# Performance work log

Measured on AMD Instinct MI355X. Metric: run time of the kernel, lower is better.

The kernel has to match this reference:

```python
import jax, jax.numpy as jnp
import numpy as np

WEIGHT_SP = 0.1
BANDWIDTH = 0.5
EPS = 1e-5


def _l2_normalize(v, axis, eps=1e-12):
    # matches torch F.normalize(p=2): x / max(||x||, eps)
    n = jnp.sqrt(jnp.sum(v * v, axis=axis, keepdims=True))
    return v / jnp.maximum(n, eps)


def _compute_meshgrid(N, H, W):
    rows = jnp.arange(H, dtype=jnp.float32) / (H + 1)
    cols = jnp.arange(W, dtype=jnp.float32) / (W + 1)
    gr, gc = jnp.meshgrid(rows, cols, indexing="ij")
    grid = jnp.stack([gr, gc])[None]  # (1, 2, H, W)
    return jnp.broadcast_to(grid, (N, 2, H, W))


def _l2_distance(x, y):
    # Faithful to the torch code; its broadcasting is only valid for N == 1.
    N, C, H, W = x.shape
    xv = x.reshape(N, C, -1)
    yv = y.reshape(N, C, -1)
    x_s = jnp.sum(xv ** 2, axis=1)          # (N, HW)
    y_s = jnp.sum(yv ** 2, axis=1)          # (N, HW)
    A = jnp.einsum("nci,ncj->nij", yv, xv)  # (N, HW, HW)
    dist = y_s - 2.0 * A + x_s.T            # same broadcast as torch (N==1)
    dist = jnp.swapaxes(dist, 1, 2)         # transpose(1,2); reshape is no-op
    return jnp.maximum(dist, 0.0)


def _cosine_distance(x, y):
    y_mu = jnp.mean(y, axis=(0, 2, 3), keepdims=True)   # (1, C, 1, 1)
    xn = _l2_normalize(x - y_mu, axis=1)
    yn = _l2_normalize(y - y_mu, axis=1)
    N, C = x.shape[:2]
    xn = xn.reshape(N, C, -1)
    yn = yn.reshape(N, C, -1)
    cos = jnp.einsum("nci,ncj->nij", xn, yn)            # (N, HW, HW)
    return 1.0 - cos


def _relative_distance(dist, eps=1e-5):
    dmin = jnp.min(dist, axis=2, keepdims=True)
    return dist / (dmin + eps)


def _compute_cx(dist_tilde, bandwidth):
    w = jnp.exp((1.0 - dist_tilde) / bandwidth)
    return w / jnp.sum(w, axis=2, keepdims=True)


def setup_inputs() -> dict:
    key = jax.random.key(0)
    k1, k2 = jax.random.split(key)
    x = jax.random.normal(k1, (1, 512, 80, 80), dtype=jnp.float32)
    y = jax.random.normal(k2, (1, 512, 80, 80), dtype=jnp.float32)
    return {"x": x, "y": y}


def reference(x, y):
    N, C, H, W = x.shape
    # spatial branch
    grid = _compute_meshgrid(N, H, W)
    cx_sp = _compute_cx(_relative_distance(_l2_distance(grid, grid), 1e-5), BANDWIDTH)
    # feature branch (loss_type == 'cosine')
    cx_feat = _compute_cx(_relative_distance(_cosine_distance(x, y), EPS), BANDWIDTH)
    cx_combine = (1.0 - WEIGHT_SP) * cx_feat + WEIGHT_SP * cx_sp
    k_max = jnp.max(cx_combine, axis=2, keepdims=True)  # (N, HW, 1)
    cx = jnp.mean(k_max, axis=1)                        # (N, 1)
    return jnp.mean(-jnp.log(cx + EPS))
```

## Files before the change

kernel.cpp:

```cpp
#include <hip/hip_runtime.h>
#include <hip/hip_bf16.h>
#include <math.h>

#define HW 6400
#define NC 512
#define NH 80
#define NW 80
#define NCH 25
#define NSLOT 50
#define NCYS 8
#define JCH 256
#define TI 128
#define BK 64
#define NT16 400

typedef __attribute__((ext_vector_type(8))) short short8;
typedef __attribute__((ext_vector_type(4))) float v4f;

#define MU_OFF    0
#define SQX_OFF   512
#define SQY_OFF   (512 + HW)
#define ACC_OFF   (512 + 2*HW)
#define GMAXP_OFF (ACC_OFF + 64)
#define INVD_OFF  (GMAXP_OFF + HW*NSLOT)
#define ZP_OFF    (INVD_OFF + HW)
#define WDP_OFF   (ZP_OFF + HW*NSLOT)
#define F32_FLOATS (WDP_OFF + HW*NCYS)
#define XB_BYTE   ((size_t)(((F32_FLOATS*4) + 255) & ~255))
#define YB_BYTE   (XB_BYTE + (size_t)HW*NC*2)
#define G_BYTE    (YB_BYTE + (size_t)HW*NC*2)
#define G_BYTES   ((size_t)NT16 * NT16 * 256 * 2)

typedef __attribute__((address_space(1))) unsigned int uint_g;
typedef __attribute__((address_space(3))) unsigned int uint_l;
__device__ __forceinline__ void gload16(const void* g, void* l) {
    __builtin_amdgcn_global_load_lds((const uint_g*)g, (uint_l*)l, 16, 0, 0);
}

__global__ void k_mu(const float* __restrict__ y, float* __restrict__ mu) {
    int c = blockIdx.x;
    const float* yc = y + (size_t)c * HW;
    float s = 0.f;
    for (int i = threadIdx.x; i < HW; i += 256) s += yc[i];
    __shared__ float red[256];
    red[threadIdx.x] = s;
    __syncthreads();
    for (int off = 128; off > 0; off >>= 1) {
        if (threadIdx.x < off) red[threadIdx.x] += red[threadIdx.x + off];
        __syncthreads();
    }
    if (threadIdx.x == 0) mu[c] = red[0] * (1.0f / HW);
}

__global__ void k_transpose(const float* __restrict__ x, const float* __restrict__ y,
                            const float* __restrict__ mu,
                            float* __restrict__ sqx, float* __restrict__ sqy,
                            unsigned short* __restrict__ xb, unsigned short* __restrict__ yb) {
    __shared__ float tile[64 * 68];
    const int t = threadIdx.x;
    const int i0 = blockIdx.x * 64;
    const int c0 = blockIdx.y * 64;
    const int z = blockIdx.z;
    const float* src = z ? y : x;
    float* sq = z ? sqy : sqx;
    unsigned short* dst = z ? yb : xb;

    #pragma unroll 4
    for (int it = 0; it < 16; ++it) {
        int cl = it * 4 + (t >> 6);
        int il = t & 63;
        float v = src[(size_t)(c0 + cl) * HW + i0 + il] - mu[c0 + cl];
        tile[il * 68 + cl] = v;
    }
    __syncthreads();
    {
        int il = t & 63, q = t >> 6;
        float s = 0.f;
        #pragma unroll
        for (int cl = q * 16; cl < q * 16 + 16; ++cl) {
            float v = tile[il * 68 + cl];
            s = fmaf(v, v, s);
        }
        atomicAdd(&sq[i0 + il], s);
    }
    #pragma unroll
    for (int it = 0; it < 2; ++it) {
        int il = t >> 2;
        int seg = (t & 3) + it * 4;
        unsigned int pk[4];
        #pragma unroll
        for (int p = 0; p < 4; ++p) {
            float v0 = tile[il * 68 + seg * 8 + p * 2];
            float v1 = tile[il * 68 + seg * 8 + p * 2 + 1];
            __hip_bfloat16 h0 = __float2bfloat16(v0);
            __hip_bfloat16 h1 = __float2bfloat16(v1);
            unsigned short u0 = *reinterpret_cast<unsigned short*>(&h0);
            unsigned short u1 = *reinterpret_cast<unsigned short*>(&h1);
            pk[p] = (unsigned int)u0 | ((unsigned int)u1 << 16);
        }
        uint4 val = make_uint4(pk[0], pk[1], pk[2], pk[3]);
        *(uint4*)&dst[(size_t)(i0 + il) * NC + c0 + seg * 8] = val;
    }
}

__global__ void k_normfin(float* __restrict__ sqx, float* __restrict__ sqy) {
    int i = blockIdx.x * 256 + threadIdx.x;
    sqx[i] = 1.0f / fmaxf(sqrtf(sqx[i]), 1e-12f);
    sqy[i] = 1.0f / fmaxf(sqrtf(sqy[i]), 1e-12f);
}

__device__ __forceinline__ void rmax_epilogue(float (&rmax)[16], float* gmaxp,
                                              int i0, int wr, int wc, int lr, int lg) {
    #pragma unroll
    for (int u = 0; u < 16; ++u) {
        float v = rmax[u];
        v = fmaxf(v, __shfl_xor(v, 1));
        v = fmaxf(v, __shfl_xor(v, 2));
        v = fmaxf(v, __shfl_xor(v, 4));
        v = fmaxf(v, __shfl_xor(v, 8));
        if (lr == 0) {
            int row = i0 + wr * 64 + (u >> 2) * 16 + lg * 4 + (u & 3);
            gmaxp[(size_t)row * NSLOT + blockIdx.y * 2 + wc] = v;
        }
    }
}

__global__ __launch_bounds__(256, 2) void k_pass1s(const unsigned short* __restrict__ Xb,
                                                   const unsigned short* __restrict__ Yb,
                                                   const float* __restrict__ sxi,
                                                   const float* __restrict__ syi,
                                                   float* __restrict__ gmaxp,
                                                   unsigned int* __restrict__ G2) {
    __shared__ char sA[128 * 128];
    __shared__ char sB[256 * 128];
    const int t = threadIdx.x;
    const int w = t >> 6, l = t & 63;
    const int wr = w >> 1, wc = w & 1;
    const int lr = l & 15, lg = l >> 4;
    const int i0 = blockIdx.x * TI;
    const int jbase = blockIdx.y * JCH;

    int aoff[4][2], boff[8][2];
    #pragma unroll
    for (int mt = 0; mt < 4; ++mt) {
        int row = wr * 64 + mt * 16 + lr;
        #pragma unroll
        for (int ks = 0; ks < 2; ++ks) {
            int seg = ks * 4 + lg;
            aoff[mt][ks] = row * 128 + ((seg ^ (row & 7)) * 16);
        }
    }
    #pragma unroll
    for (int nt = 0; nt < 8; ++nt) {
        int row = wc * 128 + nt * 16 + lr;
        #pragma unroll
        for (int ks = 0; ks < 2; ++ks) {
            int seg = ks * 4 + lg;
            boff[nt][ks] = row * 128 + ((seg ^ (row & 7)) * 16);
        }
    }

    const int strow = l >> 3;
    const int stcol = ((l & 7) ^ strow) * 8;
    const unsigned short* ga = Xb + (size_t)(i0 + w * 32 + strow) * NC + stcol;
    const unsigned short* gb = Yb + (size_t)(jbase + w * 64 + strow) * NC + stcol;
    char* dA = sA + w * 4096;
    char* dB = sB + w * 8192;

    v4f acc[4][8];
    #pragma unroll
    for (int mt = 0; mt < 4; ++mt)
        #pragma unroll
        for (int nt = 0; nt < 8; ++nt)
            acc[mt][nt] = (v4f){0.f, 0.f, 0.f, 0.f};

    #pragma unroll 1
    for (int kt = 0; kt < NC; kt += BK) {
        __syncthreads();
        gload16(ga + kt,           dA);
        gload16(ga + 8  * NC + kt, dA + 1024);
        gload16(ga + 16 * NC + kt, dA + 2048);
        gload16(ga + 24 * NC + kt, dA + 3072);
        #pragma unroll
        for (int it = 0; it < 8; ++it)
            gload16(gb + it * 8 * NC + kt, dB + it * 1024);
        __syncthreads();
        #pragma unroll
        for (int ks = 0; ks < 2; ++ks) {
            short8 af[4], bf[8];
            #pragma unroll
            for (int mt = 0; mt < 4; ++mt) af[mt] = *(const short8*)&sA[aoff[mt][ks]];
            #pragma unroll
            for (int nt = 0; nt < 8; ++nt) bf[nt] = *(const short8*)&sB[boff[nt][ks]];
            #pragma unroll
            for (int mt = 0; mt < 4; ++mt)
                #pragma unroll
                for (int nt = 0; nt < 8; ++nt)
                    acc[mt][nt] = __builtin_amdgcn_mfma_f32_16x16x32_bf16(
                        af[mt], bf[nt], acc[mt][nt], 0, 0, 0);
        }
    }

    float rsx[16];
    #pragma unroll
    for (int u = 0; u < 16; ++u) {
        int row = i0 + wr * 64 + (u >> 2) * 16 + lg * 4 + (u & 3);
        rsx[u] = sxi[row];
    }
    float rsy[8];
    #pragma unroll
    for (int nt = 0; nt < 8; ++nt)
        rsy[nt] = syi[jbase + wc * 128 + nt * 16 + lr];

    float rmax[16];
    #pragma unroll
    for (int u = 0; u < 16; ++u) rmax[u] = -3.0e38f;

    #pragma unroll
    for (int mt = 0; mt < 4; ++mt) {
        size_t rbase = (size_t)(i0 / 16 + wr * 4 + mt) * (NT16 * 128);
        #pragma unroll
        for (int nt = 0; nt < 8; ++nt) {
            int ct = jbase / 16 + wc * 8 + nt;
            float g0 = acc[mt][nt][0] * rsx[mt * 4 + 0] * rsy[nt];
            float g1 = acc[mt][nt][1] * rsx[mt * 4 + 1] * rsy[nt];
            float g2 = acc[mt][nt][2] * rsx[mt * 4 + 2] * rsy[nt];
            float g3 = acc[mt][nt][3] * rsx[mt * 4 + 3] * rsy[nt];
            rmax[mt * 4 + 0] = fmaxf(rmax[mt * 4 + 0], g0);
            rmax[mt * 4 + 1] = fmaxf(rmax[mt * 4 + 1], g1);
            rmax[mt * 4 + 2] = fmaxf(rmax[mt * 4 + 2], g2);
            rmax[mt * 4 + 3] = fmaxf(rmax[mt * 4 + 3], g3);
            __hip_bfloat16 h0 = __float2bfloat16(g0);
            __hip_bfloat16 h1 = __float2bfloat16(g1);
            __hip_bfloat16 h2 = __float2bfloat16(g2);
            __hip_bfloat16 h3 = __float2bfloat16(g3);
            unsigned int pk0 = (unsigned int)*(unsigned short*)&h0 | ((unsigned int)*(unsigned short*)&h1 << 16);
            unsigned int pk1 = (unsigned int)*(unsigned short*)&h2 | ((unsigned int)*(unsigned short*)&h3 << 16);
            *(uint2*)&G2[rbase + (size_t)ct * 128 + l * 2] = make_uint2(pk0, pk1);
        }
    }
    rmax_epilogue(rmax, gmaxp, i0, wr, wc, lr, lg);
}

__global__ __launch_bounds__(256) void k_pass2s(const unsigned int* __restrict__ G2,
                                                const float* __restrict__ gmaxp,
                                                float* __restrict__ zp,
                                                float* __restrict__ wdp) {
    const int t = threadIdx.x;
    const int w = t >> 6, l = t & 63;
    const int lr = l & 15, lg = l >> 4;
    const int rt = blockIdx.x * 4 + w;
    const int cy = blockIdx.y;

    float m = -3.0e38f;
    {
        int row = rt * 16 + lr;
        #pragma unroll
        for (int k = 0; k < 13; ++k) {
            int s = lg + 4 * k;
            if (s < NSLOT) m = fmaxf(m, gmaxp[(size_t)row * NSLOT + s]);
        }
        m = fmaxf(m, __shfl_xor(m, 16));
        m = fmaxf(m, __shfl_xor(m, 32));
    }
    float inv_lr = 1.0f / ((1.0f - m) + 1e-5f);
    float c1[4], c2[4];
    #pragma unroll
    for (int r = 0; r < 4; ++r) {
        float iv = __shfl(inv_lr, lg * 4 + r);
        c2[r] = 2.0f * iv;
        c1[r] = 2.0f - 2.0f * iv;
    }

    const uint2* base = (const uint2*)G2 + (size_t)rt * (NT16 * 64) + l;
    float zs[4] = {0.f, 0.f, 0.f, 0.f};
    #pragma unroll 4
    for (int ct = cy * 50; ct < cy * 50 + 50; ++ct) {
        uint2 v = base[(size_t)ct * 64];
        float g0 = __uint_as_float((v.x & 0xFFFFu) << 16);
        float g1 = __uint_as_float(v.x & 0xFFFF0000u);
        float g2 = __uint_as_float((v.y & 0xFFFFu) << 16);
        float g3 = __uint_as_float(v.y & 0xFFFF0000u);
        zs[0] += __expf(fmaf(c2[0], g0, c1[0]));
        zs[1] += __expf(fmaf(c2[1], g1, c1[1]));
        zs[2] += __expf(fmaf(c2[2], g2, c1[2]));
        zs[3] += __expf(fmaf(c2[3], g3, c1[3]));
    }
    float wd[4] = {0.f, 0.f, 0.f, 0.f};
    if (rt / 50 == cy) {
        uint2 v = base[(size_t)rt * 64];
        float g[4];
        g[0] = __uint_as_float((v.x & 0xFFFFu) << 16);
        g[1] = __uint_as_float(v.x & 0xFFFF0000u);
        g[2] = __uint_as_float((v.y & 0xFFFFu) << 16);
        g[3] = __uint_as_float(v.y & 0xFFFF0000u);
        #pragma unroll
        for (int r = 0; r < 4; ++r)
            if (lr == lg * 4 + r) wd[r] = __expf(fmaf(c2[r], g[r], c1[r]));
    }
    #pragma unroll
    for (int r = 0; r < 4; ++r) {
        float z = zs[r], d = wd[r];
        z += __shfl_xor(z, 1);  d += __shfl_xor(d, 1);
        z += __shfl_xor(z, 2);  d += __shfl_xor(d, 2);
        z += __shfl_xor(z, 4);  d += __shfl_xor(d, 4);
        z += __shfl_xor(z, 8);  d += __shfl_xor(d, 8);
        if (lr == 0) {
            int row = rt * 16 + lg * 4 + r;
            zp[(size_t)row * NCYS + cy] = z;
            wdp[(size_t)row * NCYS + cy] = d;
        }
    }
}

__global__ void k_kmax_s(const float* __restrict__ zp, const float* __restrict__ wdp,
                         const float* __restrict__ gmaxp, float* __restrict__ accum,
                         int* __restrict__ counter, float* __restrict__ out) {
    int i = blockIdx.x * 256 + threadIdx.x;
    float Z = 0.f, wd = 0.f, gmax = -3.0e38f;
    #pragma unroll
    for (int s = 0; s < NCYS; ++s) {
        Z += zp[(size_t)i * NCYS + s];
        wd += wdp[(size_t)i * NCYS + s];
    }
    #pragma unroll
    for (int s = 0; s < NSLOT; ++s) gmax = fmaxf(gmax, gmaxp[(size_t)i * NSLOT + s]);
    float dmin = 1.0f - gmax;
    float inv = 1.0f / (dmin + 1e-5f);
    float wmx = __expf(2.0f - 2.0f * dmin * inv);
    float invZ = 1.0f / Z;
    float kmax = fmaxf(0.9f * wmx * invZ, 0.9f * wd * invZ + 0.1f);

    __shared__ float red[256];
    red[threadIdx.x] = kmax;
    __syncthreads();
    for (int off = 128; off > 0; off >>= 1) {
        if (threadIdx.x < off) red[threadIdx.x] += red[threadIdx.x + off];
        __syncthreads();
    }
    if (threadIdx.x == 0) {
        atomicAdd(accum, red[0]);
        __threadfence();
        int n = atomicAdd(counter, 1);
        if (n == (int)gridDim.x - 1) {
            float total = atomicAdd(accum, 0.0f);
            out[0] = -logf(total * (1.0f / HW) + 1e-5f);
        }
    }
}

template <typename F>
__device__ __forceinline__ void gemm_driver(const unsigned short* __restrict__ Xb,
                                            const unsigned short* __restrict__ Yb,
                                            F&& consume) {
    __shared__ char sA[TI * BK * 2];
    __shared__ char sB[TI * BK * 2];
    const int t = threadIdx.x;
    const int w = t >> 6, l = t & 63;
    const int wr = w >> 1, wc = w & 1;
    const int lr = l & 15, lg = l >> 4;
    const int i0 = blockIdx.x * TI;
    const int jbase = blockIdx.y * JCH;

    int aoff[4][2], boff[4][2];
    #pragma unroll
    for (int mt = 0; mt < 4; ++mt) {
        int row = wr * 64 + mt * 16 + lr;
        #pragma unroll
        for (int ks = 0; ks < 2; ++ks) {
            int seg = ks * 4 + lg;
            aoff[mt][ks] = row * 128 + ((seg ^ (row & 7)) * 16);
        }
    }
    #pragma unroll
    for (int nt = 0; nt < 4; ++nt) {
        int row = wc * 64 + nt * 16 + lr;
        #pragma unroll
        for (int ks = 0; ks < 2; ++ks) {
            int seg = ks * 4 + lg;
            boff[nt][ks] = row * 128 + ((seg ^ (row & 7)) * 16);
        }
    }
    const int strow = l >> 3;
    const int stcol = ((l & 7) ^ strow) * 8;
    char* dA0 = sA + (w * 4 + 0) * 1024;
    char* dA1 = sA + (w * 4 + 1) * 1024;
    char* dA2 = sA + (w * 4 + 2) * 1024;
    char* dA3 = sA + (w * 4 + 3) * 1024;
    char* dB0 = sB + (w * 4 + 0) * 1024;
    char* dB1 = sB + (w * 4 + 1) * 1024;
    char* dB2 = sB + (w * 4 + 2) * 1024;
    char* dB3 = sB + (w * 4 + 3) * 1024;
    const unsigned short* ga = Xb + (size_t)(i0 + w * 32 + strow) * NC + stcol;
    const unsigned short* gb0 = Yb + (size_t)(jbase + w * 32 + strow) * NC + stcol;

    #pragma unroll 1
    for (int jt = 0; jt < JCH; jt += TI) {
        const unsigned short* gb = gb0 + (size_t)jt * NC;
        v4f acc[4][4];
        #pragma unroll
        for (int mt = 0; mt < 4; ++mt)
            #pragma unroll
            for (int nt = 0; nt < 4; ++nt)
                acc[mt][nt] = (v4f){0.f, 0.f, 0.f, 0.f};

        #pragma unroll 1
        for (int kt = 0; kt < NC; kt += BK) {
            __syncthreads();
            gload16(ga + kt,           dA0);
            gload16(ga + 8  * NC + kt, dA1);
            gload16(ga + 16 * NC + kt, dA2);
            gload16(ga + 24 * NC + kt, dA3);
            gload16(gb + kt,           dB0);
            gload16(gb + 8  * NC + kt, dB1);
            gload16(gb + 16 * NC + kt, dB2);
            gload16(gb + 24 * NC + kt, dB3);
            __syncthreads();
            #pragma unroll
            for (int ks = 0; ks < 2; ++ks) {
                short8 af[4], bf[4];
                #pragma unroll
                for (int mt = 0; mt < 4; ++mt) af[mt] = *(const short8*)&sA[aoff[mt][ks]];
                #pragma unroll
                for (int nt = 0; nt < 4; ++nt) bf[nt] = *(const short8*)&sB[boff[nt][ks]];
                #pragma unroll
                for (int mt = 0; mt < 4; ++mt)
                    #pragma unroll
                    for (int nt = 0; nt < 4; ++nt)
                        acc[mt][nt] = __builtin_amdgcn_mfma_f32_16x16x32_bf16(
                            af[mt], bf[nt], acc[mt][nt], 0, 0, 0);
            }
        }
        consume(acc, jt);
    }
}

__global__ __launch_bounds__(256, 2) void k_pass1(const unsigned short* __restrict__ Xb,
                                                  const unsigned short* __restrict__ Yb,
                                                  const float* __restrict__ sxi,
                                                  const float* __restrict__ syi,
                                                  float* __restrict__ gmaxp) {
    const int t = threadIdx.x;
    const int w = t >> 6, l = t & 63;
    const int wr = w >> 1, wc = w & 1;
    const int lr = l & 15, lg = l >> 4;
    const int i0 = blockIdx.x * TI;
    const int jbase = blockIdx.y * JCH;
    float rsx[16], rmax[16];
    #pragma unroll
    for (int u = 0; u < 16; ++u) {
        int row = i0 + wr * 64 + (u >> 2) * 16 + lg * 4 + (u & 3);
        rsx[u] = sxi[row];
        rmax[u] = -3.0e38f;
    }
    gemm_driver(Xb, Yb, [&](v4f (&acc)[4][4], int jt) {
        #pragma unroll
        for (int nt = 0; nt < 4; ++nt) {
            float sy = syi[jbase + jt + (wc * 4 + nt) * 16 + lr];
            #pragma unroll
            for (int mt = 0; mt < 4; ++mt)
                #pragma unroll
                for (int r = 0; r < 4; ++r)
                    rmax[mt * 4 + r] = fmaxf(rmax[mt * 4 + r],
                                             acc[mt][nt][r] * rsx[mt * 4 + r] * sy);
        }
    });
    rmax_epilogue(rmax, gmaxp, i0, wr, wc, lr, lg);
}

__global__ void k_invd(const float* __restrict__ gmaxp, float* __restrict__ invd) {
    int i = blockIdx.x * 256 + threadIdx.x;
    float m = -3.0e38f;
    #pragma unroll
    for (int s = 0; s < NSLOT; ++s) m = fmaxf(m, gmaxp[(size_t)i * NSLOT + s]);
    invd[i] = 1.0f / ((1.0f - m) + 1e-5f);
}

__global__ __launch_bounds__(256, 2) void k_pass2(const unsigned short* __restrict__ Xb,
                                                  const unsigned short* __restrict__ Yb,
                                                  const float* __restrict__ sxi,
                                                  const float* __restrict__ syi,
                                                  const float* __restrict__ invd,
                                                  float* __restrict__ zp) {
    const int t = threadIdx.x;
    const int w = t >> 6, l = t & 63;
    const int wr = w >> 1, wc = w & 1;
    const int lr = l & 15, lg = l >> 4;
    const int i0 = blockIdx.x * TI;
    const int jbase = blockIdx.y * JCH;
    float zs[16], c1[16], c2[16], rsx[16];
    #pragma unroll
    for (int u = 0; u < 16; ++u) {
        int row = i0 + wr * 64 + (u >> 2) * 16 + lg * 4 + (u & 3);
        float inv = invd[row];
        c2[u] = 2.0f * inv;
        c1[u] = 2.0f - 2.0f * inv;
        rsx[u] = sxi[row];
        zs[u] = 0.f;
    }
    gemm_driver(Xb, Yb, [&](v4f (&acc)[4][4], int jt) {
        #pragma unroll
        for (int nt = 0; nt < 4; ++nt) {
            float sy = syi[jbase + jt + (wc * 4 + nt) * 16 + lr];
            #pragma unroll
            for (int mt = 0; mt < 4; ++mt)
                #pragma unroll
                for (int r = 0; r < 4; ++r) {
                    int u = mt * 4 + r;
                    float g = acc[mt][nt][r] * rsx[u] * sy;
                    zs[u] += __expf(fmaf(c2[u], g, c1[u]));
                }
        }
    });
    #pragma unroll
    for (int u = 0; u < 16; ++u) {
        float z = zs[u];
        z += __shfl_xor(z, 1);
        z += __shfl_xor(z, 2);
        z += __shfl_xor(z, 4);
        z += __shfl_xor(z, 8);
        if (lr == 0) {
            int row = i0 + wr * 64 + (u >> 2) * 16 + lg * 4 + (u & 3);
            zp[(size_t)row * NSLOT + blockIdx.y * 2 + wc] = z;
        }
    }
}

__global__ void k_kmax(const float* __restrict__ zp, const float* __restrict__ gmaxp,
                       const unsigned short* __restrict__ Xb, const unsigned short* __restrict__ Yb,
                       const float* __restrict__ sxi, const float* __restrict__ syi,
                       float* __restrict__ accum, int* __restrict__ counter,
                       float* __restrict__ out) {
    int i = blockIdx.x * 256 + threadIdx.x;
    float Z = 0.f, gmax = -3.0e38f;
    #pragma unroll
    for (int s = 0; s < NSLOT; ++s) {
        Z += zp[(size_t)i * NSLOT + s];
        gmax = fmaxf(gmax, gmaxp[(size_t)i * NSLOT + s]);
    }
    float gii = 0.f;
    const uint2* xr = (const uint2*)(Xb + (size_t)i * NC);
    const uint2* yr = (const uint2*)(Yb + (size_t)i * NC);
    for (int c4 = 0; c4 < NC / 4; ++c4) {
        uint2 xa = xr[c4], ya = yr[c4];
        float x0 = __uint_as_float((xa.x & 0xFFFFu) << 16), y0 = __uint_as_float((ya.x & 0xFFFFu) << 16);
        float x1 = __uint_as_float(xa.x & 0xFFFF0000u),     y1 = __uint_as_float(ya.x & 0xFFFF0000u);
        float x2 = __uint_as_float((xa.y & 0xFFFFu) << 16), y2 = __uint_as_float((ya.y & 0xFFFFu) << 16);
        float x3 = __uint_as_float(xa.y & 0xFFFF0000u),     y3 = __uint_as_float(ya.y & 0xFFFF0000u);
        gii = fmaf(x0, y0, gii); gii = fmaf(x1, y1, gii);
        gii = fmaf(x2, y2, gii); gii = fmaf(x3, y3, gii);
    }
    gii *= sxi[i] * syi[i];
    float dmin = 1.0f - gmax;
    float inv = 1.0f / (dmin + 1e-5f);
    float wmx = __expf(2.0f - 2.0f * dmin * inv);
    float wii = __expf(2.0f - 2.0f * (1.0f - gii) * inv);
    float invZ = 1.0f / Z;
    float kmax = fmaxf(0.9f * wmx * invZ, 0.9f * wii * invZ + 0.1f);

    __shared__ float red[256];
    red[threadIdx.x] = kmax;
    __syncthreads();
    for (int off = 128; off > 0; off >>= 1) {
        if (threadIdx.x < off) red[threadIdx.x] += red[threadIdx.x + off];
        __syncthreads();
    }
    if (threadIdx.x == 0) {
        atomicAdd(accum, red[0]);
        __threadfence();
        int n = atomicAdd(counter, 1);
        if (n == (int)gridDim.x - 1) {
            float total = atomicAdd(accum, 0.0f);
            out[0] = -logf(total * (1.0f / HW) + 1e-5f);
        }
    }
}

extern "C" void kernel_launch(void* const* d_in, const int* in_sizes, int n_in,
                              void* d_out, int out_size, void* d_ws, size_t ws_size,
                              hipStream_t stream) {
    const float* x = (const float*)d_in[0];
    const float* y = (const float*)d_in[1];
    float* out = (float*)d_out;
    float* ws = (float*)d_ws;

    float* mu    = ws + MU_OFF;
    float* sqx   = ws + SQX_OFF;
    float* sqy   = ws + SQY_OFF;
    float* accum = ws + ACC_OFF;
    int*   counter = (int*)(accum + 1);
    float* gmaxp = ws + GMAXP_OFF;
    float* invd  = ws + INVD_OFF;
    float* zp    = ws + ZP_OFF;
    float* wdp   = ws + WDP_OFF;
    unsigned short* Xb = (unsigned short*)((char*)d_ws + XB_BYTE);
    unsigned short* Yb = (unsigned short*)((char*)d_ws + YB_BYTE);
    unsigned int*   G2 = (unsigned int*)((char*)d_ws + G_BYTE);

    const bool bigws = ws_size >= (G_BYTE + G_BYTES);

    hipMemsetAsync(sqx, 0, (2 * HW + 64) * sizeof(float), stream);

    hipLaunchKernelGGL(k_mu, dim3(NC), dim3(256), 0, stream, y, mu);
    hipLaunchKernelGGL(k_transpose, dim3(HW / 64, NC / 64, 2), dim3(256), 0, stream,
                       x, y, mu, sqx, sqy, Xb, Yb);
    hipLaunchKernelGGL(k_normfin, dim3(HW / 256), dim3(256), 0, stream, sqx, sqy);

    dim3 grid(HW / TI, NCH);
    if (bigws) {
        hipLaunchKernelGGL(k_pass1s, grid, dim3(256), 0, stream, Xb, Yb, sqx, sqy, gmaxp, G2);
        hipLaunchKernelGGL(k_pass2s, dim3(NT16 / 4, NCYS), dim3(256), 0, stream, G2, gmaxp, zp, wdp);
        hipLaunchKernelGGL(k_kmax_s, dim3(HW / 256), dim3(256), 0, stream, zp, wdp, gmaxp,
                           accum, counter, out);
    } else {
        hipLaunchKernelGGL(k_pass1, grid, dim3(256), 0, stream, Xb, Yb, sqx, sqy, gmaxp);
        hipLaunchKernelGGL(k_invd, dim3(HW / 256), dim3(256), 0, stream, gmaxp, invd);
        hipLaunchKernelGGL(k_pass2, grid, dim3(256), 0, stream, Xb, Yb, sqx, sqy, invd, zp);
        hipLaunchKernelGGL(k_kmax, dim3(HW / 256), dim3(256), 0, stream, zp, gmaxp, Xb, Yb,
                           sqx, sqy, accum, counter, out);
    }
}
```

Baseline: 164.1 us.

## Store normalized Gram matrix in FP8 and fold norm finalization into GEMM

The stored similarity matrix drops from packed bf16 to packed fp8 (e4m3), halving the bytes pass1s writes and pass2s reads. The diagonal is written separately at fp32 so pass2s no longer has to compute a diagonal term. The norm-finalization kernel is removed and reciprocal norms are computed inline from the squared sums. pass1s is reworked to a 128x128 tile looped over the 256-column chunk, with launch bounds raised to 3 blocks per CU. The cost is fp8 rounding error inside the exponentials of the softmax denominator, which may hurt accuracy.

Measured after the change: 168.0 us. 2.3% more time.

```diff
diff --git a/kernel.cpp b/kernel.cpp
--- a/kernel.cpp
+++ b/kernel.cpp
@@ -22,19 +22,22 @@
 #define SQY_OFF   (512 + HW)
 #define ACC_OFF   (512 + 2*HW)
 #define GMAXP_OFF (ACC_OFF + 64)
-#define INVD_OFF  (GMAXP_OFF + HW*NSLOT)
-#define ZP_OFF    (INVD_OFF + HW)
-#define WDP_OFF   (ZP_OFF + HW*NSLOT)
-#define F32_FLOATS (WDP_OFF + HW*NCYS)
+#define GDIAG_OFF (GMAXP_OFF + HW*NSLOT)
+#define ZP_OFF    (GDIAG_OFF + HW)
+#define F32_FLOATS (ZP_OFF + HW*NSLOT)
 #define XB_BYTE   ((size_t)(((F32_FLOATS*4) + 255) & ~255))
 #define YB_BYTE   (XB_BYTE + (size_t)HW*NC*2)
 #define G_BYTE    (YB_BYTE + (size_t)HW*NC*2)
-#define G_BYTES   ((size_t)NT16 * NT16 * 256 * 2)
+#define G_BYTES   ((size_t)NT16 * NT16 * 256)
 
 typedef __attribute__((address_space(1))) unsigned int uint_g;
 typedef __attribute__((address_space(3))) unsigned int uint_l;
 __device__ __forceinline__ void gload16(const void* g, void* l) {
     __builtin_amdgcn_global_load_lds((const uint_g*)g, (uint_l*)l, 16, 0, 0);
+}
+
+__device__ __forceinline__ float rnorm_of(float sq) {
+    return 1.0f / fmaxf(sqrtf(sq), 1e-12f);
 }
 
 __global__ void k_mu(const float* __restrict__ y, float* __restrict__ mu) {
@@ -103,12 +106,6 @@
     }
 }
 
-__global__ void k_normfin(float* __restrict__ sqx, float* __restrict__ sqy) {
-    int i = blockIdx.x * 256 + threadIdx.x;
-    sqx[i] = 1.0f / fmaxf(sqrtf(sqx[i]), 1e-12f);
-    sqy[i] = 1.0f / fmaxf(sqrtf(sqy[i]), 1e-12f);
-}
-
 __device__ __forceinline__ void rmax_epilogue(float (&rmax)[16], float* gmaxp,
                                               int i0, int wr, int wc, int lr, int lg) {
     #pragma unroll
@@ -125,234 +122,13 @@
     }
 }
 
-__global__ __launch_bounds__(256, 2) void k_pass1s(const unsigned short* __restrict__ Xb,
+__global__ __launch_bounds__(256, 3) void k_pass1s(const unsigned short* __restrict__ Xb,
                                                    const unsigned short* __restrict__ Yb,
-                                                   const float* __restrict__ sxi,
-                                                   const float* __restrict__ syi,
+                                                   const float* __restrict__ sqx,
+                                                   const float* __restrict__ sqy,
                                                    float* __restrict__ gmaxp,
-                                                   unsigned int* __restrict__ G2) {
-    __shared__ char sA[128 * 128];
-    __shared__ char sB[256 * 128];
-    const int t = threadIdx.x;
-    const int w = t >> 6, l = t & 63;
-    const int wr = w >> 1, wc = w & 1;
-    const int lr = l & 15, lg = l >> 4;
-    const int i0 = blockIdx.x * TI;
-    const int jbase = blockIdx.y * JCH;
-
-    int aoff[4][2], boff[8][2];
-    #pragma unroll
-    for (int mt = 0; mt < 4; ++mt) {
-        int row = wr * 64 + mt * 16 + lr;
-        #pragma unroll
-        for (int ks = 0; ks < 2; ++ks) {
-            int seg = ks * 4 + lg;
-            aoff[mt][ks] = row * 128 + ((seg ^ (row & 7)) * 16);
-        }
-    }
-    #pragma unroll
-    for (int nt = 0; nt < 8; ++nt) {
-        int row = wc * 128 + nt * 16 + lr;
-        #pragma unroll
-        for (int ks = 0; ks < 2; ++ks) {
-            int seg = ks * 4 + lg;
-            boff[nt][ks] = row * 128 + ((seg ^ (row & 7)) * 16);
-        }
-    }
-
-    const int strow = l >> 3;
-    const int stcol = ((l & 7) ^ strow) * 8;
-    const unsigned short* ga = Xb + (size_t)(i0 + w * 32 + strow) * NC + stcol;
-    const unsigned short* gb = Yb + (size_t)(jbase + w * 64 + strow) * NC + stcol;
-    char* dA = sA + w * 4096;
-    char* dB = sB + w * 8192;
-
-    v4f acc[4][8];
-    #pragma unroll
-    for (int mt = 0; mt < 4; ++mt)
-        #pragma unroll
-        for (int nt = 0; nt < 8; ++nt)
-            acc[mt][nt] = (v4f){0.f, 0.f, 0.f, 0.f};
-
-    #pragma unroll 1
-    for (int kt = 0; kt < NC; kt += BK) {
-        __syncthreads();
-        gload16(ga + kt,           dA);
-        gload16(ga + 8  * NC + kt, dA + 1024);
-        gload16(ga + 16 * NC + kt, dA + 2048);
-        gload16(ga + 24 * NC + kt, dA + 3072);
-        #pragma unroll
-        for (int it = 0; it < 8; ++it)
-            gload16(gb + it * 8 * NC + kt, dB + it * 1024);
-        __syncthreads();
-        #pragma unroll
-        for (int ks = 0; ks < 2; ++ks) {
-            short8 af[4], bf[8];
-            #pragma unroll
-            for (int mt = 0; mt < 4; ++mt) af[mt] = *(const short8*)&sA[aoff[mt][ks]];
-            #pragma unroll
-            for (int nt = 0; nt < 8; ++nt) bf[nt] = *(const short8*)&sB[boff[nt][ks]];
-            #pragma unroll
-            for (int mt = 0; mt < 4; ++mt)
-                #pragma unroll
-                for (int nt = 0; nt < 8; ++nt)
-                    acc[mt][nt] = __builtin_amdgcn_mfma_f32_16x16x32_bf16(
-                        af[mt], bf[nt], acc[mt][nt], 0, 0, 0);
-        }
-    }
-
-    float rsx[16];
-    #pragma unroll
-    for (int u = 0; u < 16; ++u) {
-        int row = i0 + wr * 64 + (u >> 2) * 16 + lg * 4 + (u & 3);
-        rsx[u] = sxi[row];
-    }
-    float rsy[8];
-    #pragma unroll
-    for (int nt = 0; nt < 8; ++nt)
-        rsy[nt] = syi[jbase + wc * 128 + nt * 16 + lr];
-
-    float rmax[16];
-    #pragma unroll
-    for (int u = 0; u < 16; ++u) rmax[u] = -3.0e38f;
-
-    #pragma unroll
-    for (int mt = 0; mt < 4; ++mt) {
-        size_t rbase = (size_t)(i0 / 16 + wr * 4 + mt) * (NT16 * 128);
-        #pragma unroll
-        for (int nt = 0; nt < 8; ++nt) {
-            int ct = jbase / 16 + wc * 8 + nt;
-            float g0 = acc[mt][nt][0] * rsx[mt * 4 + 0] * rsy[nt];
-            float g1 = acc[mt][nt][1] * rsx[mt * 4 + 1] * rsy[nt];
-            float g2 = acc[mt][nt][2] * rsx[mt * 4 + 2] * rsy[nt];
-            float g3 = acc[mt][nt][3] * rsx[mt * 4 + 3] * rsy[nt];
-            rmax[mt * 4 + 0] = fmaxf(rmax[mt * 4 + 0], g0);
-            rmax[mt * 4 + 1] = fmaxf(rmax[mt * 4 + 1], g1);
-            rmax[mt * 4 + 2] = fmaxf(rmax[mt * 4 + 2], g2);
-            rmax[mt * 4 + 3] = fmaxf(rmax[mt * 4 + 3], g3);
-            __hip_bfloat16 h0 = __float2bfloat16(g0);
-            __hip_bfloat16 h1 = __float2bfloat16(g1);
-            __hip_bfloat16 h2 = __float2bfloat16(g2);
-            __hip_bfloat16 h3 = __float2bfloat16(g3);
-            unsigned int pk0 = (unsigned int)*(unsigned short*)&h0 | ((unsigned int)*(unsigned short*)&h1 << 16);
-            unsigned int pk1 = (unsigned int)*(unsigned short*)&h2 | ((unsigned int)*(unsigned short*)&h3 << 16);
-            *(uint2*)&G2[rbase + (size_t)ct * 128 + l * 2] = make_uint2(pk0, pk1);
-        }
-    }
-    rmax_epilogue(rmax, gmaxp, i0, wr, wc, lr, lg);
-}
-
-__global__ __launch_bounds__(256) void k_pass2s(const unsigned int* __restrict__ G2,
-                                                const float* __restrict__ gmaxp,
-                                                float* __restrict__ zp,
-                                                float* __restrict__ wdp) {
-    const int t = threadIdx.x;
-    const int w = t >> 6, l = t & 63;
-    const int lr = l & 15, lg = l >> 4;
-    const int rt = blockIdx.x * 4 + w;
-    const int cy = blockIdx.y;
-
-    float m = -3.0e38f;
-    {
-        int row = rt * 16 + lr;
-        #pragma unroll
-        for (int k = 0; k < 13; ++k) {
-            int s = lg + 4 * k;
-            if (s < NSLOT) m = fmaxf(m, gmaxp[(size_t)row * NSLOT + s]);
-        }
-        m = fmaxf(m, __shfl_xor(m, 16));
-        m = fmaxf(m, __shfl_xor(m, 32));
-    }
-    float inv_lr = 1.0f / ((1.0f - m) + 1e-5f);
-    float c1[4], c2[4];
-    #pragma unroll
-    for (int r = 0; r < 4; ++r) {
-        float iv = __shfl(inv_lr, lg * 4 + r);
-        c2[r] = 2.0f * iv;
-        c1[r] = 2.0f - 2.0f * iv;
-    }
-
-    const uint2* base = (const uint2*)G2 + (size_t)rt * (NT16 * 64) + l;
-    float zs[4] = {0.f, 0.f, 0.f, 0.f};
-    #pragma unroll 4
-    for (int ct = cy * 50; ct < cy * 50 + 50; ++ct) {
-        uint2 v = base[(size_t)ct * 64];
-        float g0 = __uint_as_float((v.x & 0xFFFFu) << 16);
-        float g1 = __uint_as_float(v.x & 0xFFFF0000u);
-        float g2 = __uint_as_float((v.y & 0xFFFFu) << 16);
-        float g3 = __uint_as_float(v.y & 0xFFFF0000u);
-        zs[0] += __expf(fmaf(c2[0], g0, c1[0]));
-        zs[1] += __expf(fmaf(c2[1], g1, c1[1]));
-        zs[2] += __expf(fmaf(c2[2], g2, c1[2]));
-        zs[3] += __expf(fmaf(c2[3], g3, c1[3]));
-    }
-    float wd[4] = {0.f, 0.f, 0.f, 0.f};
-    if (rt / 50 == cy) {
-        uint2 v = base[(size_t)rt * 64];
-        float g[4];
-        g[0] = __uint_as_float((v.x & 0xFFFFu) << 16);
-        g[1] = __uint_as_float(v.x & 0xFFFF0000u);
-        g[2] = __uint_as_float((v.y & 0xFFFFu) << 16);
-        g[3] = __uint_as_float(v.y & 0xFFFF0000u);
-        #pragma unroll
-        for (int r = 0; r < 4; ++r)
-            if (lr == lg * 4 + r) wd[r] = __expf(fmaf(c2[r], g[r], c1[r]));
-    }
-    #pragma unroll
-    for (int r = 0; r < 4; ++r) {
-        float z = zs[r], d = wd[r];
-        z += __shfl_xor(z, 1);  d += __shfl_xor(d, 1);
-        z += __shfl_xor(z, 2);  d += __shfl_xor(d, 2);
-        z += __shfl_xor(z, 4);  d += __shfl_xor(d, 4);
-        z += __shfl_xor(z, 8);  d += __shfl_xor(d, 8);
-        if (lr == 0) {
-            int row = rt * 16 + lg * 4 + r;
-            zp[(size_t)row * NCYS + cy] = z;
-            wdp[(size_t)row * NCYS + cy] = d;
-        }
-    }
-}
-
-__global__ void k_kmax_s(const float* __restrict__ zp, const float* __restrict__ wdp,
-                         const float* __restrict__ gmaxp, float* __restrict__ accum,
-                         int* __restrict__ counter, float* __restrict__ out) {
-    int i = blockIdx.x * 256 + threadIdx.x;
-    float Z = 0.f, wd = 0.f, gmax = -3.0e38f;
-    #pragma unroll
-    for (int s = 0; s < NCYS; ++s) {
-        Z += zp[(size_t)i * NCYS + s];
-        wd += wdp[(size_t)i * NCYS + s];
-    }
-    #pragma unroll
-    for (int s = 0; s < NSLOT; ++s) gmax = fmaxf(gmax, gmaxp[(size_t)i * NSLOT + s]);
-    float dmin = 1.0f - gmax;
-    float inv = 1.0f / (dmin + 1e-5f);
-    float wmx = __expf(2.0f - 2.0f * dmin * inv);
-    float invZ = 1.0f / Z;
-    float kmax = fmaxf(0.9f * wmx * invZ, 0.9f * wd * invZ + 0.1f);
-
-    __shared__ float red[256];
-    red[threadIdx.x] = kmax;
-    __syncthreads();
-    for (int off = 128; off > 0; off >>= 1) {
-        if (threadIdx.x < off) red[threadIdx.x] += red[threadIdx.x + off];
-        __syncthreads();
-    }
-    if (threadIdx.x == 0) {
-        atomicAdd(accum, red[0]);
-        __threadfence();
-        int n = atomicAdd(counter, 1);
-        if (n == (int)gridDim.x - 1) {
-            float total = atomicAdd(accum, 0.0f);
-            out[0] = -logf(total * (1.0f / HW) + 1e-5f);
-        }
-    }
-}
-
-template <typename F>
-__device__ __forceinline__ void gemm_driver(const unsigned short* __restrict__ Xb,
-                                            const unsigned short* __restrict__ Yb,
-                                            F&& consume) {
+                                                   float* __restrict__ gdiag,
+                                                   unsigned int* __restrict__ G1) {
     __shared__ char sA[TI * BK * 2];
     __shared__ char sB[TI * BK * 2];
     const int t = threadIdx.x;
@@ -393,6 +169,16 @@
     char* dB3 = sB + (w * 4 + 3) * 1024;
     const unsigned short* ga = Xb + (size_t)(i0 + w * 32 + strow) * NC + stcol;
     const unsigned short* gb0 = Yb + (size_t)(jbase + w * 32 + strow) * NC + stcol;
+
+    float rsx[16];
+    #pragma unroll
+    for (int u = 0; u < 16; ++u) {
+        int row = i0 + wr * 64 + (u >> 2) * 16 + lg * 4 + (u & 3);
+        rsx[u] = rnorm_of(sqx[row]);
+    }
+    float rmax[16];
+    #pragma unroll
+    for (int u = 0; u < 16; ++u) rmax[u] = -3.0e38f;
 
     #pragma unroll 1
     for (int jt = 0; jt < JCH; jt += TI) {
@@ -431,14 +217,218 @@
                             af[mt], bf[nt], acc[mt][nt], 0, 0, 0);
             }
         }
+
+        #pragma unroll
+        for (int nt = 0; nt < 4; ++nt) {
+            int col = jbase + jt + wc * 64 + nt * 16 + lr;
+            float sy = rnorm_of(sqy[col]);
+            int ct = col >> 4;
+            #pragma unroll
+            for (int mt = 0; mt < 4; ++mt) {
+                int rowb = i0 + wr * 64 + mt * 16 + lg * 4;
+                float g0 = acc[mt][nt][0] * rsx[mt * 4 + 0] * sy;
+                float g1 = acc[mt][nt][1] * rsx[mt * 4 + 1] * sy;
+                float g2 = acc[mt][nt][2] * rsx[mt * 4 + 2] * sy;
+                float g3 = acc[mt][nt][3] * rsx[mt * 4 + 3] * sy;
+                rmax[mt * 4 + 0] = fmaxf(rmax[mt * 4 + 0], g0);
+                rmax[mt * 4 + 1] = fmaxf(rmax[mt * 4 + 1], g1);
+                rmax[mt * 4 + 2] = fmaxf(rmax[mt * 4 + 2], g2);
+                rmax[mt * 4 + 3] = fmaxf(rmax[mt * 4 + 3], g3);
+                unsigned int pk = __builtin_amdgcn_cvt_pk_fp8_f32(g0, g1, 0, false);
+                pk = __builtin_amdgcn_cvt_pk_fp8_f32(g2, g3, pk, true);
+                size_t rbase = (size_t)(i0 / 16 + wr * 4 + mt) * (NT16 * 64);
+                G1[rbase + (size_t)ct * 64 + l] = pk;
+                if (col == rowb + 0) gdiag[col] = g0;
+                if (col == rowb + 1) gdiag[col] = g1;
+                if (col == rowb + 2) gdiag[col] = g2;
+                if (col == rowb + 3) gdiag[col] = g3;
+            }
+        }
+    }
+    rmax_epilogue(rmax, gmaxp, i0, wr, wc, lr, lg);
+}
+
+__global__ __launch_bounds__(256) void k_pass2s(const unsigned int* __restrict__ G1,
+                                                const float* __restrict__ gmaxp,
+                                                float* __restrict__ zp) {
+    const int t = threadIdx.x;
+    const int w = t >> 6, l = t & 63;
+    const int lr = l & 15, lg = l >> 4;
+    const int rt = blockIdx.x * 4 + w;
+    const int cy = blockIdx.y;
+
+    float m = -3.0e38f;
+    {
+        int row = rt * 16 + lr;
+        #pragma unroll
+        for (int k = 0; k < 13; ++k) {
+            int s = lg + 4 * k;
+            if (s < NSLOT) m = fmaxf(m, gmaxp[(size_t)row * NSLOT + s]);
+        }
+        m = fmaxf(m, __shfl_xor(m, 16));
+        m = fmaxf(m, __shfl_xor(m, 32));
+    }
+    float inv_lr = 1.0f / ((1.0f - m) + 1e-5f);
+    float c1[4], c2[4];
+    #pragma unroll
+    for (int r = 0; r < 4; ++r) {
+        float iv = __shfl(inv_lr, lg * 4 + r);
+        c2[r] = 2.0f * iv;
+        c1[r] = 2.0f - 2.0f * iv;
+    }
+
+    const unsigned int* base = G1 + (size_t)rt * (NT16 * 64) + l;
+    float zs[4] = {0.f, 0.f, 0.f, 0.f};
+    #pragma unroll 4
+    for (int ct = cy * 50; ct < cy * 50 + 50; ++ct) {
+        unsigned int v = base[(size_t)ct * 64];
+        float g0 = __builtin_amdgcn_cvt_f32_fp8(v, 0);
+        float g1 = __builtin_amdgcn_cvt_f32_fp8(v, 1);
+        float g2 = __builtin_amdgcn_cvt_f32_fp8(v, 2);
+        float g3 = __builtin_amdgcn_cvt_f32_fp8(v, 3);
+        zs[0] += __expf(fmaf(c2[0], g0, c1[0]));
+        zs[1] += __expf(fmaf(c2[1], g1, c1[1]));
+        zs[2] += __expf(fmaf(c2[2], g2, c1[2]));
+        zs[3] += __expf(fmaf(c2[3], g3, c1[3]));
+    }
+    #pragma unroll
+    for (int r = 0; r < 4; ++r) {
+        float z = zs[r];
+        z += __shfl_xor(z, 1);
+        z += __shfl_xor(z, 2);
+        z += __shfl_xor(z, 4);
+        z += __shfl_xor(z, 8);
+        if (lr == 0) {
+            int row = rt * 16 + lg * 4 + r;
+            zp[(size_t)row * NCYS + cy] = z;
+        }
+    }
+}
+
+__global__ void k_kmax_s(const float* __restrict__ zp, const float* __restrict__ gdiag,
+                         const float* __restrict__ gmaxp, float* __restrict__ accum,
+                         int* __restrict__ counter, float* __restrict__ out) {
+    int i = blockIdx.x * 256 + threadIdx.x;
+    float Z = 0.f, gmax = -3.0e38f;
+    #pragma unroll
+    for (int s = 0; s < NCYS; ++s) Z += zp[(size_t)i * NCYS + s];
+    #pragma unroll
+    for (int s = 0; s < NSLOT; ++s) gmax = fmaxf(gmax, gmaxp[(size_t)i * NSLOT + s]);
+    float dmin = 1.0f - gmax;
+    float inv = 1.0f / (dmin + 1e-5f);
+    float wmx = __expf(2.0f - 2.0f * dmin * inv);
+    float wii = __expf(2.0f - 2.0f * (1.0f - gdiag[i]) * inv);
+    float invZ = 1.0f / Z;
+    float kmax = fmaxf(0.9f * wmx * invZ, 0.9f * wii * invZ + 0.1f);
+
+    __shared__ float red[256];
+    red[threadIdx.x] = kmax;
+    __syncthreads();
+    for (int off = 128; off > 0; off >>= 1) {
+        if (threadIdx.x < off) red[threadIdx.x] += red[threadIdx.x + off];
+        __syncthreads();
+    }
+    if (threadIdx.x == 0) {
+        atomicAdd(accum, red[0]);
+        __threadfence();
+        int n = atomicAdd(counter, 1);
+        if (n == (int)gridDim.x - 1) {
+            float total = atomicAdd(accum, 0.0f);
+            out[0] = -logf(total * (1.0f / HW) + 1e-5f);
+        }
+    }
+}
+
+template <typename F>
+__device__ __forceinline__ void gemm_driver(const unsigned short* __restrict__ Xb,
+                                            const unsigned short* __restrict__ Yb,
+                                            F&& consume) {
+    __shared__ char sA[TI * BK * 2];
+    __shared__ char sB[TI * BK * 2];
+    const int t = threadIdx.x;
+    const int w = t >> 6, l = t & 63;
+    const int wr = w >> 1, wc = w & 1;
+    const int lr = l & 15, lg = l >> 4;
+    const int i0 = blockIdx.x * TI;
+    const int jbase = blockIdx.y * JCH;
+
+    int aoff[4][2], boff[4][2];
+    #pragma unroll
+    for (int mt = 0; mt < 4; ++mt) {
+        int row = wr * 64 + mt * 16 + lr;
+        #pragma unroll
+        for (int ks = 0; ks < 2; ++ks) {
+            int seg = ks * 4 + lg;
+            aoff[mt][ks] = row * 128 + ((seg ^ (row & 7)) * 16);
+        }
+    }
+    #pragma unroll
+    for (int nt = 0; nt < 4; ++nt) {
+        int row = wc * 64 + nt * 16 + lr;
+        #pragma unroll
+        for (int ks = 0; ks < 2; ++ks) {
+            int seg = ks * 4 + lg;
+            boff[nt][ks] = row * 128 + ((seg ^ (row & 7)) * 16);
+        }
+    }
+    const int strow = l >> 3;
+    const int stcol = ((l & 7) ^ strow) * 8;
+    char* dA0 = sA + (w * 4 + 0) * 1024;
+    char* dA1 = sA + (w * 4 + 1) * 1024;
+    char* dA2 = sA + (w * 4 + 2) * 1024;
+    char* dA3 = sA + (w * 4 + 3) * 1024;
+    char* dB0 = sB + (w * 4 + 0) * 1024;
+    char* dB1 = sB + (w * 4 + 1) * 1024;
+    char* dB2 = sB + (w * 4 + 2) * 1024;
+    char* dB3 = sB + (w * 4 + 3) * 1024;
+    const unsigned short* ga = Xb + (size_t)(i0 + w * 32 + strow) * NC + stcol;
+    const unsigned short* gb0 = Yb + (size_t)(jbase + w * 32 + strow) * NC + stcol;
+
+    #pragma unroll 1
+    for (int jt = 0; jt < JCH; jt += TI) {
+        const unsigned short* gb = gb0 + (size_t)jt * NC;
+        v4f acc[4][4];
+        #pragma unroll
+        for (int mt = 0; mt < 4; ++mt)
+            #pragma unroll
+            for (int nt = 0; nt < 4; ++nt)
+                acc[mt][nt] = (v4f){0.f, 0.f, 0.f, 0.f};
+
+        #pragma unroll 1
+        for (int kt = 0; kt < NC; kt += BK) {
+            __syncthreads();
+            gload16(ga + kt,           dA0);
+            gload16(ga + 8  * NC + kt, dA1);
+            gload16(ga + 16 * NC + kt, dA2);
+            gload16(ga + 24 * NC + kt, dA3);
+            gload16(gb + kt,           dB0);
+            gload16(gb + 8  * NC + kt, dB1);
+            gload16(gb + 16 * NC + kt, dB2);
+            gload16(gb + 24 * NC + kt, dB3);
+            __syncthreads();
+            #pragma unroll
+            for (int ks = 0; ks < 2; ++ks) {
+                short8 af[4], bf[4];
+                #pragma unroll
+                for (int mt = 0; mt < 4; ++mt) af[mt] = *(const short8*)&sA[aoff[mt][ks]];
+                #pragma unroll
+                for (int nt = 0; nt < 4; ++nt) bf[nt] = *(const short8*)&sB[boff[nt][ks]];
+                #pragma unroll
+                for (int mt = 0; mt < 4; ++mt)
+                    #pragma unroll
+                    for (int nt = 0; nt < 4; ++nt)
+                        acc[mt][nt] = __builtin_amdgcn_mfma_f32_16x16x32_bf16(
+                            af[mt], bf[nt], acc[mt][nt], 0, 0, 0);
+            }
+        }
         consume(acc, jt);
     }
 }
 
 __global__ __launch_bounds__(256, 2) void k_pass1(const unsigned short* __restrict__ Xb,
                                                   const unsigned short* __restrict__ Yb,
-                                                  const float* __restrict__ sxi,
-                                                  const float* __restrict__ syi,
+                                                  const float* __restrict__ sqx,
+                                                  const float* __restrict__ sqy,
                                                   float* __restrict__ gmaxp) {
     const int t = threadIdx.x;
     const int w = t >> 6, l = t & 63;
@@ -450,13 +440,13 @@
     #pragma unroll
     for (int u = 0; u < 16; ++u) {
         int row = i0 + wr * 64 + (u >> 2) * 16 + lg * 4 + (u & 3);
-        rsx[u] = sxi[row];
+        rsx[u] = rnorm_of(sqx[row]);
         rmax[u] = -3.0e38f;
     }
     gemm_driver(Xb, Yb, [&](v4f (&acc)[4][4], int jt) {
         #pragma unroll
         for (int nt = 0; nt < 4; ++nt) {
-            float sy = syi[jbase + jt + (wc * 4 + nt) * 16 + lr];
+            float sy = rnorm_of(sqy[jbase + jt + (wc * 4 + nt) * 16 + lr]);
             #pragma unroll
             for (int mt = 0; mt < 4; ++mt)
                 #pragma unroll
@@ -478,8 +468,8 @@
 
 __global__ __launch_bounds__(256, 2) void k_pass2(const unsigned short* __restrict__ Xb,
                                                   const unsigned short* __restrict__ Yb,
-                                                  const float* __restrict__ sxi,
-                                                  const float* __restrict__ syi,
+                                                  const float* __restrict__ sqx,
+                                                  const float* __restrict__ sqy,
                                                   const float* __restrict__ invd,
                                                   float* __restrict__ zp) {
     const int t = threadIdx.x;
@@ -495,13 +485,13 @@
         float inv = invd[row];
         c2[u] = 2.0f * inv;
         c1[u] = 2.0f - 2.0f * inv;
-        rsx[u] = sxi[row];
+        rsx[u] = rnorm_of(sqx[row]);
         zs[u] = 0.f;
     }
     gemm_driver(Xb, Yb, [&](v4f (&acc)[4][4], int jt) {
         #pragma unroll
         for (int nt = 0; nt < 4; ++nt) {
-            float sy = syi[jbase + jt + (wc * 4 + nt) * 16 + lr];
+            float sy = rnorm_of(sqy[jbase + jt + (wc * 4 + nt) * 16 + lr]);
             #pragma unroll
             for (int mt = 0; mt < 4; ++mt)
                 #pragma unroll
@@ -528,7 +518,7 @@
 
 __global__ void k_kmax(const float* __restrict__ zp, const float* __restrict__ gmaxp,
                        const unsigned short* __restrict__ Xb, const unsigned short* __restrict__ Yb,
-                       const float* __restrict__ sxi, const float* __restrict__ syi,
+                       const float* __restrict__ sqx, const float* __restrict__ sqy,
                        float* __restrict__ accum, int* __restrict__ counter,
                        float* __restrict__ out) {
     int i = blockIdx.x * 256 + threadIdx.x;
@@ -550,7 +540,7 @@
         gii = fmaf(x0, y0, gii); gii = fmaf(x1, y1, gii);
         gii = fmaf(x2, y2, gii); gii = fmaf(x3, y3, gii);
     }
-    gii *= sxi[i] * syi[i];
+    gii *= rnorm_of(sqx[i]) * rnorm_of(sqy[i]);
     float dmin = 1.0f - gmax;
     float inv = 1.0f / (dmin + 1e-5f);
     float wmx = __expf(2.0f - 2.0f * dmin * inv);
@@ -590,12 +580,11 @@
     float* accum = ws + ACC_OFF;
     int*   counter = (int*)(accum + 1);
     float* gmaxp = ws + GMAXP_OFF;
-    float* invd  = ws + INVD_OFF;
+    float* gdiag = ws + GDIAG_OFF;
     float* zp    = ws + ZP_OFF;
-    float* wdp   = ws + WDP_OFF;
     unsigned short* Xb = (unsigned short*)((char*)d_ws + XB_BYTE);
     unsigned short* Yb = (unsigned short*)((char*)d_ws + YB_BYTE);
-    unsigned int*   G2 = (unsigned int*)((char*)d_ws + G_BYTE);
+    unsigned int*   G1 = (unsigned int*)((char*)d_ws + G_BYTE);
 
     const bool bigws = ws_size >= (G_BYTE + G_BYTES);
 
@@ -604,18 +593,18 @@
     hipLaunchKernelGGL(k_mu, dim3(NC), dim3(256), 0, stream, y, mu);
     hipLaunchKernelGGL(k_transpose, dim3(HW / 64, NC / 64, 2), dim3(256), 0, stream,
                        x, y, mu, sqx, sqy, Xb, Yb);
-    hipLaunchKernelGGL(k_normfin, dim3(HW / 256), dim3(256), 0, stream, sqx, sqy);
 
     dim3 grid(HW / TI, NCH);
     if (bigws) {
-        hipLaunchKernelGGL(k_pass1s, grid, dim3(256), 0, stream, Xb, Yb, sqx, sqy, gmaxp, G2);
-        hipLaunchKernelGGL(k_pass2s, dim3(NT16 / 4, NCYS), dim3(256), 0, stream, G2, gmaxp, zp, wdp);
-        hipLaunchKernelGGL(k_kmax_s, dim3(HW / 256), dim3(256), 0, stream, zp, wdp, gmaxp,
+        hipLaunchKernelGGL(k_pass1s, grid, dim3(256), 0, stream, Xb, Yb, sqx, sqy,
+                           gmaxp, gdiag, G1);
+        hipLaunchKernelGGL(k_pass2s, dim3(NT16 / 4, NCYS), dim3(256), 0, stream, G1, gmaxp, zp);
+        hipLaunchKernelGGL(k_kmax_s, dim3(HW / 256), dim3(256), 0, stream, zp, gdiag, gmaxp,
                            accum, counter, out);
     } else {
         hipLaunchKernelGGL(k_pass1, grid, dim3(256), 0, stream, Xb, Yb, sqx, sqy, gmaxp);
-        hipLaunchKernelGGL(k_invd, dim3(HW / 256), dim3(256), 0, stream, gmaxp, invd);
-        hipLaunchKernelGGL(k_pass2, grid, dim3(256), 0, stream, Xb, Yb, sqx, sqy, invd, zp);
+        hipLaunchKernelGGL(k_invd, dim3(HW / 256), dim3(256), 0, stream, gmaxp, gdiag);
+        hipLaunchKernelGGL(k_pass2, grid, dim3(256), 0, stream, Xb, Yb, sqx, sqy, gdiag, zp);
         hipLaunchKernelGGL(k_kmax, dim3(HW / 256), dim3(256), 0, stream, zp, gmaxp, Xb, Yb,
                            sqx, sqy, accum, counter, out);
     }
```
